# Kernel tuning notes

Hardware: AMD Instinct MI355X
Metric: run time of the kernel (lower is better)

## Reference

```python
import jax, jax.numpy as jnp
import numpy as np

BN_EPS = 1e-5

def _binarize(x):
    # sign with STE semantics (Binarize on .data in torch => identity grad)
    b = jnp.where(x >= 0, 1.0, -1.0).astype(x.dtype)
    return x + jax.lax.stop_gradient(b - x)

def _bin_linear(x, w, b, binarize_input):
    xb = _binarize(x) if binarize_input else x
    wb = _binarize(w)
    return xb @ wb.T + b

def _bn(x, g, be, m, v):
    return (x - m) * (g * jax.lax.rsqrt(v + BN_EPS)) + be

def _hardtanh(x):
    return jnp.clip(x, -1.0, 1.0)

def setup_inputs() -> dict:
    key = jax.random.key(0)
    ks = jax.random.split(key, 8)
    B, D_in, H, D_out = 16384, 784, 4096, 10
    inp = {
        'x':  jax.random.normal(ks[0], (B, D_in), jnp.float32),
        'w1': jax.random.normal(ks[1], (H, D_in), jnp.float32) * 0.05,
        'b1': jax.random.normal(ks[2], (H,), jnp.float32) * 0.05,
        'g1': jnp.ones((H,), jnp.float32), 'be1': jnp.zeros((H,), jnp.float32),
        'm1': jnp.zeros((H,), jnp.float32), 'v1': jnp.ones((H,), jnp.float32),
        'w2': jax.random.normal(ks[3], (H, H), jnp.float32) * 0.05,
        'b2': jax.random.normal(ks[4], (H,), jnp.float32) * 0.05,
        'g2': jnp.ones((H,), jnp.float32), 'be2': jnp.zeros((H,), jnp.float32),
        'm2': jnp.zeros((H,), jnp.float32), 'v2': jnp.ones((H,), jnp.float32),
        'w3': jax.random.normal(ks[5], (H, H), jnp.float32) * 0.05,
        'b3': jax.random.normal(ks[6], (H,), jnp.float32) * 0.05,
        'g3': jnp.ones((H,), jnp.float32), 'be3': jnp.zeros((H,), jnp.float32),
        'm3': jnp.zeros((H,), jnp.float32), 'v3': jnp.ones((H,), jnp.float32),
        'w4': jax.random.normal(ks[7], (D_out, H), jnp.float32) * 0.05,
        'b4': jnp.zeros((D_out,), jnp.float32),
    }
    return inp

def reference(x, w1, b1, g1, be1, m1, v1,
              w2, b2, g2, be2, m2, v2,
              w3, b3, g3, be3, m3, v3,
              w4, b4):
    # eval mode: BN uses running stats, dropout is identity
    h = _bin_linear(x.reshape(-1, w1.shape[1]), w1, b1, binarize_input=False)
    h = _hardtanh(_bn(h, g1, be1, m1, v1))
    h = _bin_linear(h, w2, b2, binarize_input=True)
    h = _hardtanh(_bn(h, g2, be2, m2, v2))
    h = _bin_linear(h, w3, b3, binarize_input=True)
    h = _hardtanh(_bn(h, g3, be3, m3, v3))
    h = _bin_linear(h, w4, b4, binarize_input=True)
    return jax.nn.log_softmax(h, axis=1)
```

## Files before the change

kernel.cpp:

```cpp
#include <hip/hip_runtime.h>
#include <stdint.h>
#include <math.h>

#define BATCH 16384
#define DIN   784
#define HID   4096
#define DOUT  10
#define KW    128
#define BN_EPS 1e-5

constexpr size_t SZ_BITS   = (size_t)BATCH * KW * 4;
constexpr size_t OFF_BITS1 = 0;
constexpr size_t OFF_BITS2 = OFF_BITS1 + SZ_BITS;
constexpr size_t OFF_W2B   = OFF_BITS2 + SZ_BITS;
constexpr size_t OFF_W3B   = OFF_W2B + (size_t)HID * KW * 4;
constexpr size_t OFF_W4B   = OFF_W3B + (size_t)HID * KW * 4;

__global__ __launch_bounds__(256) void binarize_kernel(
    const float* __restrict__ w, uint32_t* __restrict__ bits, int nwords) {
  int t = blockIdx.x * 256 + threadIdx.x;
  if (t >= nwords) return;
  const float* p = w + (size_t)t * 32;
  uint32_t word = 0;
#pragma unroll
  for (int q = 0; q < 8; ++q) {
    float4 v = *(const float4*)(p + q * 4);
    word |= (uint32_t)(v.x >= 0.f) << (4 * q + 0);
    word |= (uint32_t)(v.y >= 0.f) << (4 * q + 1);
    word |= (uint32_t)(v.z >= 0.f) << (4 * q + 2);
    word |= (uint32_t)(v.w >= 0.f) << (4 * q + 3);
  }
  bits[t] = word;
}

__global__ __launch_bounds__(256) void gemm1_kernel(
    const float* __restrict__ X, const float* __restrict__ W,
    const float* __restrict__ Bv, const float* __restrict__ Gv,
    const float* __restrict__ BEv, const float* __restrict__ Mv,
    const float* __restrict__ Vv, uint32_t* __restrict__ bits_out) {
  __shared__ float As[16 * 128];
  __shared__ float Bs[16 * 128];
  __shared__ unsigned int PW[128 * 4];

  const int tid = threadIdx.x;
  const int bid = blockIdx.x;
  const int grp = bid >> 10;
  const int rem = bid & 1023;
  const int cb  = (grp << 3) + (rem & 7);
  const int rb  = rem >> 3;
  const int m0 = rb * 128, n0 = cb * 128;
  const int tx = tid & 15, ty = tid >> 4;

  float acc[8][8];
#pragma unroll
  for (int r = 0; r < 8; ++r)
#pragma unroll
    for (int c = 0; c < 8; ++c) acc[r][c] = 0.f;

  const int sr = tid >> 1;
  const int sk = (tid & 1) * 8;
  const float* xrow = X + (size_t)(m0 + sr) * DIN + sk;
  const float* wrow = W + (size_t)(n0 + sr) * DIN + sk;

  for (int k0 = 0; k0 < DIN; k0 += 16) {
    float4 a0 = *(const float4*)(xrow + k0);
    float4 a1 = *(const float4*)(xrow + k0 + 4);
    float4 b0 = *(const float4*)(wrow + k0);
    float4 b1 = *(const float4*)(wrow + k0 + 4);
    __syncthreads();
    As[(sk + 0) * 128 + sr] = a0.x;  As[(sk + 1) * 128 + sr] = a0.y;
    As[(sk + 2) * 128 + sr] = a0.z;  As[(sk + 3) * 128 + sr] = a0.w;
    As[(sk + 4) * 128 + sr] = a1.x;  As[(sk + 5) * 128 + sr] = a1.y;
    As[(sk + 6) * 128 + sr] = a1.z;  As[(sk + 7) * 128 + sr] = a1.w;
    Bs[(sk + 0) * 128 + sr] = (b0.x >= 0.f) ? 1.f : -1.f;
    Bs[(sk + 1) * 128 + sr] = (b0.y >= 0.f) ? 1.f : -1.f;
    Bs[(sk + 2) * 128 + sr] = (b0.z >= 0.f) ? 1.f : -1.f;
    Bs[(sk + 3) * 128 + sr] = (b0.w >= 0.f) ? 1.f : -1.f;
    Bs[(sk + 4) * 128 + sr] = (b1.x >= 0.f) ? 1.f : -1.f;
    Bs[(sk + 5) * 128 + sr] = (b1.y >= 0.f) ? 1.f : -1.f;
    Bs[(sk + 6) * 128 + sr] = (b1.z >= 0.f) ? 1.f : -1.f;
    Bs[(sk + 7) * 128 + sr] = (b1.w >= 0.f) ? 1.f : -1.f;
    __syncthreads();
#pragma unroll
    for (int kk = 0; kk < 16; ++kk) {
      float a[8], b[8];
      *(float4*)&a[0] = *(const float4*)&As[kk * 128 + ty * 8];
      *(float4*)&a[4] = *(const float4*)&As[kk * 128 + ty * 8 + 4];
      *(float4*)&b[0] = *(const float4*)&Bs[kk * 128 + tx * 8];
      *(float4*)&b[4] = *(const float4*)&Bs[kk * 128 + tx * 8 + 4];
#pragma unroll
      for (int r = 0; r < 8; ++r)
#pragma unroll
        for (int c = 0; c < 8; ++c)
          acc[r][c] = fmaf(a[r], b[c], acc[r][c]);
    }
  }

  uint32_t bm[8];
#pragma unroll
  for (int r = 0; r < 8; ++r) bm[r] = 0;
  for (int c = 0; c < 8; ++c) {
    const int j = n0 + tx * 8 + c;
    const double scale = (double)Gv[j] / sqrt((double)Vv[j] + BN_EPS);
    const double mj = (double)Mv[j], bej = (double)BEv[j], bj = (double)Bv[j];
#pragma unroll
    for (int r = 0; r < 8; ++r) {
      float h = acc[r][c] + (float)bj;
      double bnd = ((double)h - mj) * scale + bej;
      bm[r] |= (uint32_t)(bnd >= 0.0) << c;
    }
  }
  for (int t = tid; t < 512; t += 256) PW[t] = 0u;
  __syncthreads();
#pragma unroll
  for (int r = 0; r < 8; ++r)
    atomicOr(&PW[(ty * 8 + r) * 4 + (tx >> 2)], bm[r] << (8 * (tx & 3)));
  __syncthreads();
  for (int w = tid; w < 512; w += 256) {
    int row = w >> 2, wc = w & 3;
    bits_out[(size_t)(m0 + row) * KW + (n0 >> 5) + wc] = PW[row * 4 + wc];
  }
}

__global__ __launch_bounds__(256) void bitgemm_kernel(
    const uint32_t* __restrict__ Abits, const uint32_t* __restrict__ Wbits,
    const float* __restrict__ Bv, const float* __restrict__ Gv,
    const float* __restrict__ BEv, const float* __restrict__ Mv,
    const float* __restrict__ Vv, uint32_t* __restrict__ bits_out) {
  __shared__ uint32_t As[16 * 128];
  __shared__ uint32_t Bs[16 * 128];
  __shared__ unsigned int PW[128 * 4];

  const int tid = threadIdx.x;
  const int cb = blockIdx.x & 31, rb = blockIdx.x >> 5;
  const int m0 = rb * 128, n0 = cb * 128;
  const int tx = tid & 15, ty = tid >> 4;

  int acc[8][8];
#pragma unroll
  for (int r = 0; r < 8; ++r)
#pragma unroll
    for (int c = 0; c < 8; ++c) acc[r][c] = 0;

  const int sr = tid >> 1;
  const int sk = (tid & 1) * 8;
  const uint32_t* arow = Abits + (size_t)(m0 + sr) * KW + sk;
  const uint32_t* wrow = Wbits + (size_t)(n0 + sr) * KW + sk;

  for (int w0 = 0; w0 < KW; w0 += 16) {
    uint4 a0 = *(const uint4*)(arow + w0);
    uint4 a1 = *(const uint4*)(arow + w0 + 4);
    uint4 b0 = *(const uint4*)(wrow + w0);
    uint4 b1 = *(const uint4*)(wrow + w0 + 4);
    __syncthreads();
    As[(sk + 0) * 128 + sr] = a0.x;  As[(sk + 1) * 128 + sr] = a0.y;
    As[(sk + 2) * 128 + sr] = a0.z;  As[(sk + 3) * 128 + sr] = a0.w;
    As[(sk + 4) * 128 + sr] = a1.x;  As[(sk + 5) * 128 + sr] = a1.y;
    As[(sk + 6) * 128 + sr] = a1.z;  As[(sk + 7) * 128 + sr] = a1.w;
    Bs[(sk + 0) * 128 + sr] = b0.x;  Bs[(sk + 1) * 128 + sr] = b0.y;
    Bs[(sk + 2) * 128 + sr] = b0.z;  Bs[(sk + 3) * 128 + sr] = b0.w;
    Bs[(sk + 4) * 128 + sr] = b1.x;  Bs[(sk + 5) * 128 + sr] = b1.y;
    Bs[(sk + 6) * 128 + sr] = b1.z;  Bs[(sk + 7) * 128 + sr] = b1.w;
    __syncthreads();
#pragma unroll
    for (int kk = 0; kk < 16; ++kk) {
      uint32_t a[8], b[8];
      *(uint4*)&a[0] = *(const uint4*)&As[kk * 128 + ty * 8];
      *(uint4*)&a[4] = *(const uint4*)&As[kk * 128 + ty * 8 + 4];
      *(uint4*)&b[0] = *(const uint4*)&Bs[kk * 128 + tx * 8];
      *(uint4*)&b[4] = *(const uint4*)&Bs[kk * 128 + tx * 8 + 4];
#pragma unroll
      for (int r = 0; r < 8; ++r)
#pragma unroll
        for (int c = 0; c < 8; ++c)
          acc[r][c] += __popc(a[r] ^ b[c]);
    }
  }

  uint32_t bm[8];
#pragma unroll
  for (int r = 0; r < 8; ++r) bm[r] = 0;
  for (int c = 0; c < 8; ++c) {
    const int j = n0 + tx * 8 + c;
    const double scale = (double)Gv[j] / sqrt((double)Vv[j] + BN_EPS);
    const double mj = (double)Mv[j], bej = (double)BEv[j], bj = (double)Bv[j];
#pragma unroll
    for (int r = 0; r < 8; ++r) {
      double h = (double)(HID - 2 * acc[r][c]) + bj;
      double bnd = (h - mj) * scale + bej;
      bm[r] |= (uint32_t)(bnd >= 0.0) << c;
    }
  }
  for (int t = tid; t < 512; t += 256) PW[t] = 0u;
  __syncthreads();
#pragma unroll
  for (int r = 0; r < 8; ++r)
    atomicOr(&PW[(ty * 8 + r) * 4 + (tx >> 2)], bm[r] << (8 * (tx & 3)));
  __syncthreads();
  for (int w = tid; w < 512; w += 256) {
    int row = w >> 2, wc = w & 3;
    bits_out[(size_t)(m0 + row) * KW + (n0 >> 5) + wc] = PW[row * 4 + wc];
  }
}

__global__ __launch_bounds__(256) void final_kernel(
    const uint32_t* __restrict__ xbits, const uint32_t* __restrict__ w4b,
    const float* __restrict__ b4, float* __restrict__ out) {
  __shared__ uint32_t Ws[DOUT * KW];
  const int tid = threadIdx.x;
  for (int t = tid; t < DOUT * KW; t += 256) Ws[t] = w4b[t];
  __syncthreads();
  const int lane = tid & 63;
  const int i = blockIdx.x * 4 + (tid >> 6);
  const uint32_t x0 = xbits[(size_t)i * KW + lane];
  const uint32_t x1 = xbits[(size_t)i * KW + 64 + lane];
  int cnt[DOUT];
#pragma unroll
  for (int j = 0; j < DOUT; ++j)
    cnt[j] = __popc(x0 ^ Ws[j * KW + lane]) + __popc(x1 ^ Ws[j * KW + 64 + lane]);
#pragma unroll
  for (int j = 0; j < DOUT; ++j)
#pragma unroll
    for (int off = 32; off; off >>= 1) cnt[j] += __shfl_xor(cnt[j], off);
  double logit[DOUT];
  double mx = -1e300;
#pragma unroll
  for (int j = 0; j < DOUT; ++j) {
    logit[j] = (double)(HID - 2 * cnt[j]) + (double)b4[j];
    mx = fmax(mx, logit[j]);
  }
  double s = 0.0;
#pragma unroll
  for (int j = 0; j < DOUT; ++j) s += exp(logit[j] - mx);
  double lse = log(s) + mx;
  if (lane < DOUT)
    out[(size_t)i * DOUT + lane] = (float)(logit[lane] - lse);
}

extern "C" void kernel_launch(void* const* d_in, const int* in_sizes, int n_in,
                              void* d_out, int out_size, void* d_ws, size_t ws_size,
                              hipStream_t stream) {
  const float* x   = (const float*)d_in[0];
  const float* w1  = (const float*)d_in[1];
  const float* b1  = (const float*)d_in[2];
  const float* g1  = (const float*)d_in[3];
  const float* be1 = (const float*)d_in[4];
  const float* m1  = (const float*)d_in[5];
  const float* v1  = (const float*)d_in[6];
  const float* w2  = (const float*)d_in[7];
  const float* b2  = (const float*)d_in[8];
  const float* g2  = (const float*)d_in[9];
  const float* be2 = (const float*)d_in[10];
  const float* m2  = (const float*)d_in[11];
  const float* v2  = (const float*)d_in[12];
  const float* w3  = (const float*)d_in[13];
  const float* b3  = (const float*)d_in[14];
  const float* g3  = (const float*)d_in[15];
  const float* be3 = (const float*)d_in[16];
  const float* m3  = (const float*)d_in[17];
  const float* v3  = (const float*)d_in[18];
  const float* w4  = (const float*)d_in[19];
  const float* b4  = (const float*)d_in[20];

  char* ws = (char*)d_ws;
  uint32_t* bits1 = (uint32_t*)(ws + OFF_BITS1);
  uint32_t* bits2 = (uint32_t*)(ws + OFF_BITS2);
  uint32_t* w2b   = (uint32_t*)(ws + OFF_W2B);
  uint32_t* w3b   = (uint32_t*)(ws + OFF_W3B);
  uint32_t* w4b   = (uint32_t*)(ws + OFF_W4B);
  float*    out   = (float*)d_out;

  binarize_kernel<<<(HID * KW + 255) / 256, 256, 0, stream>>>(w2, w2b, HID * KW);
  binarize_kernel<<<(HID * KW + 255) / 256, 256, 0, stream>>>(w3, w3b, HID * KW);
  binarize_kernel<<<(DOUT * KW + 255) / 256, 256, 0, stream>>>(w4, w4b, DOUT * KW);

  gemm1_kernel<<<(BATCH / 128) * (HID / 128), 256, 0, stream>>>(
      x, w1, b1, g1, be1, m1, v1, bits1);

  bitgemm_kernel<<<(BATCH / 128) * (HID / 128), 256, 0, stream>>>(
      bits1, w2b, b2, g2, be2, m2, v2, bits2);
  bitgemm_kernel<<<(BATCH / 128) * (HID / 128), 256, 0, stream>>>(
      bits2, w3b, b3, g3, be3, m3, v3, bits1);

  final_kernel<<<BATCH / 4, 256, 0, stream>>>(bits1, w4b, b4, out);
}
```

Baseline: 2.448 ms.

## Use split-bf16 MFMA for first layer with near-threshold fp32 fixup

Replaces the scalar fp32 FMA tiling of the first layer GEMM with bf16 MFMA, splitting x into high and low bf16 parts so the product keeps near-fp32 accuracy against ±1 weights. Outputs whose BN value falls within a small margin of zero are appended to a global list through an atomic counter. A second kernel recomputes those entries exactly in fp32 and flips their sign bits where needed. The aim is to move the dominant first-layer matmul onto matrix cores. The cost is the atomics, the list capacity limit (entries beyond CAP are dropped) and a tolerance-based correctness argument.

```diff
diff --git a/kernel.cpp b/kernel.cpp
--- a/kernel.cpp
+++ b/kernel.cpp
@@ -1,4 +1,5 @@
 #include <hip/hip_runtime.h>
+#include <hip/hip_bf16.h>
 #include <stdint.h>
 #include <math.h>
 
@@ -7,7 +8,9 @@
 #define HID   4096
 #define DOUT  10
 #define KW    128
+#define CAP   1048576
 #define BN_EPS 1e-5
+#define TAU   0.05f
 
 constexpr size_t SZ_BITS   = (size_t)BATCH * KW * 4;
 constexpr size_t OFF_BITS1 = 0;
@@ -15,6 +18,25 @@
 constexpr size_t OFF_W2B   = OFF_BITS2 + SZ_BITS;
 constexpr size_t OFF_W3B   = OFF_W2B + (size_t)HID * KW * 4;
 constexpr size_t OFF_W4B   = OFF_W3B + (size_t)HID * KW * 4;
+constexpr size_t OFF_CNT   = OFF_W4B + 8192;
+constexpr size_t OFF_LIST  = OFF_CNT + 16;
+
+typedef __attribute__((ext_vector_type(8))) short frag8;
+typedef __attribute__((ext_vector_type(4))) float f32x4;
+
+__device__ __forceinline__ unsigned short f2bf_bits(float x) {
+  __hip_bfloat16 h = __float2bfloat16(x);
+  return *reinterpret_cast<unsigned short*>(&h);
+}
+__device__ __forceinline__ float bf2f(unsigned short b) {
+  union { unsigned int u; float f; } c;
+  c.u = ((unsigned int)b) << 16;
+  return c.f;
+}
+
+__global__ void zero_cnt_kernel(int* cnt) {
+  if (threadIdx.x == 0) *cnt = 0;
+}
 
 __global__ __launch_bounds__(256) void binarize_kernel(
     const float* __restrict__ w, uint32_t* __restrict__ bits, int nwords) {
@@ -33,14 +55,17 @@
   bits[t] = word;
 }
 
-__global__ __launch_bounds__(256) void gemm1_kernel(
+__global__ __launch_bounds__(256) void gemm1_mfma_kernel(
     const float* __restrict__ X, const float* __restrict__ W,
     const float* __restrict__ Bv, const float* __restrict__ Gv,
     const float* __restrict__ BEv, const float* __restrict__ Mv,
-    const float* __restrict__ Vv, uint32_t* __restrict__ bits_out) {
-  __shared__ float As[16 * 128];
-  __shared__ float Bs[16 * 128];
-  __shared__ unsigned int PW[128 * 4];
+    const float* __restrict__ Vv,
+    uint32_t* __restrict__ bits_out, int* __restrict__ cnt,
+    uint32_t* __restrict__ list) {
+  __shared__ short Ah[128 * 40];
+  __shared__ short Al[128 * 40];
+  __shared__ short Bt[128 * 40];
+  __shared__ unsigned short PW16[128 * 8];
 
   const int tid = threadIdx.x;
   const int bid = blockIdx.x;
@@ -49,76 +74,148 @@
   const int cb  = (grp << 3) + (rem & 7);
   const int rb  = rem >> 3;
   const int m0 = rb * 128, n0 = cb * 128;
-  const int tx = tid & 15, ty = tid >> 4;
-
-  float acc[8][8];
-#pragma unroll
-  for (int r = 0; r < 8; ++r)
-#pragma unroll
-    for (int c = 0; c < 8; ++c) acc[r][c] = 0.f;
-
-  const int sr = tid >> 1;
-  const int sk = (tid & 1) * 8;
-  const float* xrow = X + (size_t)(m0 + sr) * DIN + sk;
-  const float* wrow = W + (size_t)(n0 + sr) * DIN + sk;
-
-  for (int k0 = 0; k0 < DIN; k0 += 16) {
-    float4 a0 = *(const float4*)(xrow + k0);
-    float4 a1 = *(const float4*)(xrow + k0 + 4);
-    float4 b0 = *(const float4*)(wrow + k0);
-    float4 b1 = *(const float4*)(wrow + k0 + 4);
+
+  const int lane = tid & 63;
+  const int wm = (tid >> 6) & 1;
+  const int wn = tid >> 7;
+  const int l15 = lane & 15;
+  const int l4  = lane >> 4;
+
+  f32x4 acc[4][4];
+#pragma unroll
+  for (int i = 0; i < 4; ++i)
+#pragma unroll
+    for (int j = 0; j < 4; ++j) acc[i][j] = (f32x4){0.f, 0.f, 0.f, 0.f};
+
+  const int srow = tid >> 1;
+  const int skb  = (tid & 1) * 16;
+  const float* xp = X + (size_t)(m0 + srow) * DIN;
+  const float* wp = W + (size_t)(n0 + srow) * DIN;
+
+  for (int k0 = 0; k0 < 800; k0 += 32) {
+    float xv[16], wv[16];
+    const int kg = k0 + skb;
+    if (kg < DIN) {
+#pragma unroll
+      for (int q = 0; q < 4; ++q) {
+        *(float4*)&xv[q * 4] = *(const float4*)(xp + kg + q * 4);
+        *(float4*)&wv[q * 4] = *(const float4*)(wp + kg + q * 4);
+      }
+    } else {
+#pragma unroll
+      for (int e = 0; e < 16; ++e) { xv[e] = 0.f; wv[e] = 1.f; }
+    }
+    unsigned int ah[8], al[8], bt[8];
+#pragma unroll
+    for (int q = 0; q < 8; ++q) {
+      unsigned short h0 = f2bf_bits(xv[2 * q]);
+      unsigned short h1 = f2bf_bits(xv[2 * q + 1]);
+      unsigned short l0 = f2bf_bits(xv[2 * q] - bf2f(h0));
+      unsigned short l1 = f2bf_bits(xv[2 * q + 1] - bf2f(h1));
+      unsigned short s0 = (wv[2 * q] >= 0.f) ? 0x3F80u : 0xBF80u;
+      unsigned short s1 = (wv[2 * q + 1] >= 0.f) ? 0x3F80u : 0xBF80u;
+      ah[q] = (unsigned int)h0 | ((unsigned int)h1 << 16);
+      al[q] = (unsigned int)l0 | ((unsigned int)l1 << 16);
+      bt[q] = (unsigned int)s0 | ((unsigned int)s1 << 16);
+    }
     __syncthreads();
-    As[(sk + 0) * 128 + sr] = a0.x;  As[(sk + 1) * 128 + sr] = a0.y;
-    As[(sk + 2) * 128 + sr] = a0.z;  As[(sk + 3) * 128 + sr] = a0.w;
-    As[(sk + 4) * 128 + sr] = a1.x;  As[(sk + 5) * 128 + sr] = a1.y;
-    As[(sk + 6) * 128 + sr] = a1.z;  As[(sk + 7) * 128 + sr] = a1.w;
-    Bs[(sk + 0) * 128 + sr] = (b0.x >= 0.f) ? 1.f : -1.f;
-    Bs[(sk + 1) * 128 + sr] = (b0.y >= 0.f) ? 1.f : -1.f;
-    Bs[(sk + 2) * 128 + sr] = (b0.z >= 0.f) ? 1.f : -1.f;
-    Bs[(sk + 3) * 128 + sr] = (b0.w >= 0.f) ? 1.f : -1.f;
-    Bs[(sk + 4) * 128 + sr] = (b1.x >= 0.f) ? 1.f : -1.f;
-    Bs[(sk + 5) * 128 + sr] = (b1.y >= 0.f) ? 1.f : -1.f;
-    Bs[(sk + 6) * 128 + sr] = (b1.z >= 0.f) ? 1.f : -1.f;
-    Bs[(sk + 7) * 128 + sr] = (b1.w >= 0.f) ? 1.f : -1.f;
+    {
+      const int o = srow * 40 + skb;
+      *(uint4*)&Ah[o]     = *(uint4*)&ah[0];
+      *(uint4*)&Ah[o + 8] = *(uint4*)&ah[4];
+      *(uint4*)&Al[o]     = *(uint4*)&al[0];
+      *(uint4*)&Al[o + 8] = *(uint4*)&al[4];
+      *(uint4*)&Bt[o]     = *(uint4*)&bt[0];
+      *(uint4*)&Bt[o + 8] = *(uint4*)&bt[4];
+    }
     __syncthreads();
-#pragma unroll
-    for (int kk = 0; kk < 16; ++kk) {
-      float a[8], b[8];
-      *(float4*)&a[0] = *(const float4*)&As[kk * 128 + ty * 8];
-      *(float4*)&a[4] = *(const float4*)&As[kk * 128 + ty * 8 + 4];
-      *(float4*)&b[0] = *(const float4*)&Bs[kk * 128 + tx * 8];
-      *(float4*)&b[4] = *(const float4*)&Bs[kk * 128 + tx * 8 + 4];
-#pragma unroll
-      for (int r = 0; r < 8; ++r)
-#pragma unroll
-        for (int c = 0; c < 8; ++c)
-          acc[r][c] = fmaf(a[r], b[c], acc[r][c]);
-    }
-  }
-
-  uint32_t bm[8];
-#pragma unroll
-  for (int r = 0; r < 8; ++r) bm[r] = 0;
-  for (int c = 0; c < 8; ++c) {
-    const int j = n0 + tx * 8 + c;
-    const double scale = (double)Gv[j] / sqrt((double)Vv[j] + BN_EPS);
-    const double mj = (double)Mv[j], bej = (double)BEv[j], bj = (double)Bv[j];
-#pragma unroll
-    for (int r = 0; r < 8; ++r) {
-      float h = acc[r][c] + (float)bj;
-      double bnd = ((double)h - mj) * scale + bej;
-      bm[r] |= (uint32_t)(bnd >= 0.0) << c;
-    }
-  }
-  for (int t = tid; t < 512; t += 256) PW[t] = 0u;
+
+    frag8 bf[4], af_h[4], af_l[4];
+#pragma unroll
+    for (int f = 0; f < 4; ++f) {
+      bf[f]   = *(const frag8*)&Bt[(wn * 64 + f * 16 + l15) * 40 + l4 * 8];
+      af_h[f] = *(const frag8*)&Ah[(wm * 64 + f * 16 + l15) * 40 + l4 * 8];
+      af_l[f] = *(const frag8*)&Al[(wm * 64 + f * 16 + l15) * 40 + l4 * 8];
+    }
+#pragma unroll
+    for (int fm = 0; fm < 4; ++fm)
+#pragma unroll
+      for (int fn = 0; fn < 4; ++fn) {
+        acc[fm][fn] = __builtin_amdgcn_mfma_f32_16x16x32_bf16(
+            af_h[fm], bf[fn], acc[fm][fn], 0, 0, 0);
+        acc[fm][fn] = __builtin_amdgcn_mfma_f32_16x16x32_bf16(
+            af_l[fm], bf[fn], acc[fm][fn], 0, 0, 0);
+      }
+  }
+
+#pragma unroll
+  for (int fn = 0; fn < 4; ++fn) {
+    const int gj = n0 + wn * 64 + fn * 16 + l15;
+    const float  bj = Bv[gj];
+    const double scale = (double)Gv[gj] / sqrt((double)Vv[gj] + BN_EPS);
+    const double mj = (double)Mv[gj], bej = (double)BEv[gj];
+    const double thr = (double)TAU * fabs(scale);
+#pragma unroll
+    for (int fm = 0; fm < 4; ++fm) {
+#pragma unroll
+      for (int r = 0; r < 4; ++r) {
+        const int row_l = wm * 64 + fm * 16 + l4 * 4 + r;
+        float hb = acc[fm][fn][r] + bj;
+        double bnd = ((double)hb - mj) * scale + bej;
+        unsigned int bit = (bnd >= 0.0) ? 1u : 0u;
+        unsigned long long mask = __ballot(bit);
+        if (l15 == 0)
+          PW16[row_l * 8 + (wn * 4 + fn)] =
+              (unsigned short)(mask >> (l4 * 16));
+        if (fabs(bnd) < thr) {
+          int pos = atomicAdd(cnt, 1);
+          if (pos < CAP)
+            list[pos] = (uint32_t)((m0 + row_l) * HID + gj);
+        }
+      }
+    }
+  }
   __syncthreads();
-#pragma unroll
-  for (int r = 0; r < 8; ++r)
-    atomicOr(&PW[(ty * 8 + r) * 4 + (tx >> 2)], bm[r] << (8 * (tx & 3)));
-  __syncthreads();
-  for (int w = tid; w < 512; w += 256) {
-    int row = w >> 2, wc = w & 3;
-    bits_out[(size_t)(m0 + row) * KW + (n0 >> 5) + wc] = PW[row * 4 + wc];
+  for (int t = tid; t < 512; t += 256) {
+    int row = t >> 2, wc = t & 3;
+    uint32_t word = (uint32_t)PW16[row * 8 + wc * 2] |
+                    ((uint32_t)PW16[row * 8 + wc * 2 + 1] << 16);
+    bits_out[(size_t)(m0 + row) * KW + (n0 >> 5) + wc] = word;
+  }
+}
+
+__global__ __launch_bounds__(256) void fixup_chain_kernel(
+    const float* __restrict__ X, const float* __restrict__ W,
+    const float* __restrict__ Bv, const float* __restrict__ Gv,
+    const float* __restrict__ BEv, const float* __restrict__ Mv,
+    const float* __restrict__ Vv,
+    uint32_t* __restrict__ bits1, const int* __restrict__ cnt,
+    const uint32_t* __restrict__ list) {
+  int n = *cnt;
+  if (n > CAP) n = CAP;
+  for (int idx = blockIdx.x * 256 + threadIdx.x; idx < n;
+       idx += gridDim.x * 256) {
+    uint32_t code = list[idx];
+    int i = code >> 12;
+    int j = code & (HID - 1);
+    const float* xr = X + (size_t)i * DIN;
+    const float* wr = W + (size_t)j * DIN;
+    float h = 0.f;
+    for (int k = 0; k < DIN; k += 4) {
+      float4 xv = *(const float4*)(xr + k);
+      float4 wv = *(const float4*)(wr + k);
+      h = fmaf(xv.x, (wv.x >= 0.f) ? 1.f : -1.f, h);
+      h = fmaf(xv.y, (wv.y >= 0.f) ? 1.f : -1.f, h);
+      h = fmaf(xv.z, (wv.z >= 0.f) ? 1.f : -1.f, h);
+      h = fmaf(xv.w, (wv.w >= 0.f) ? 1.f : -1.f, h);
+    }
+    float hb = h + Bv[j];
+    double scale = (double)Gv[j] / sqrt((double)Vv[j] + BN_EPS);
+    double bnd = ((double)hb - (double)Mv[j]) * scale + (double)BEv[j];
+    uint32_t bit = (bnd >= 0.0) ? 1u : 0u;
+    uint32_t* wpw = &bits1[(size_t)i * KW + (j >> 5)];
+    uint32_t cur = (*wpw >> (j & 31)) & 1u;
+    if (cur != bit) atomicXor(wpw, 1u << (j & 31));
   }
 }
 
@@ -257,8 +354,8 @@
   const float* b3  = (const float*)d_in[14];
   const float* g3  = (const float*)d_in[15];
   const float* be3 = (const float*)d_in[16];
+  const float* v3  = (const float*)d_in[18];
   const float* m3  = (const float*)d_in[17];
-  const float* v3  = (const float*)d_in[18];
   const float* w4  = (const float*)d_in[19];
   const float* b4  = (const float*)d_in[20];
 
@@ -268,14 +365,19 @@
   uint32_t* w2b   = (uint32_t*)(ws + OFF_W2B);
   uint32_t* w3b   = (uint32_t*)(ws + OFF_W3B);
   uint32_t* w4b   = (uint32_t*)(ws + OFF_W4B);
+  int*      cnt   = (int*)(ws + OFF_CNT);
+  uint32_t* list  = (uint32_t*)(ws + OFF_LIST);
   float*    out   = (float*)d_out;
 
+  zero_cnt_kernel<<<1, 64, 0, stream>>>(cnt);
   binarize_kernel<<<(HID * KW + 255) / 256, 256, 0, stream>>>(w2, w2b, HID * KW);
   binarize_kernel<<<(HID * KW + 255) / 256, 256, 0, stream>>>(w3, w3b, HID * KW);
   binarize_kernel<<<(DOUT * KW + 255) / 256, 256, 0, stream>>>(w4, w4b, DOUT * KW);
 
-  gemm1_kernel<<<(BATCH / 128) * (HID / 128), 256, 0, stream>>>(
-      x, w1, b1, g1, be1, m1, v1, bits1);
+  gemm1_mfma_kernel<<<(BATCH / 128) * (HID / 128), 256, 0, stream>>>(
+      x, w1, b1, g1, be1, m1, v1, bits1, cnt, list);
+  fixup_chain_kernel<<<512, 256, 0, stream>>>(
+      x, w1, b1, g1, be1, m1, v1, bits1, cnt, list);
 
   bitgemm_kernel<<<(BATCH / 128) * (HID / 128), 256, 0, stream>>>(
       bits1, w2b, b2, g2, be2, m2, v2, bits2);
```

Result: slower. 2.507 ms (+2.4%).
